# Performance work log

Hardware: AMD Instinct MI355X
Metric: run time of the kernel (lower is better)

Reference implementation:

```python
import jax, jax.numpy as jnp
import numpy as np

B, F, H, K, E = 512, 1280, 2560, 8, 9  # batch, feat_dim, 2*feat_dim, branching, n_internal
# Tree: root=node 0 (expert 0); level-1 nodes 1..8 (experts 1..8); level-2 leaves 9..72.

def setup_inputs() -> dict:
    key = jax.random.key(0)
    k0, k1, k2, k3, k4 = jax.random.split(key, 5)
    x = jax.random.normal(k0, (B, F), dtype=jnp.float32)
    W1 = jax.random.normal(k1, (E, F, H), dtype=jnp.float32) / np.sqrt(F)
    b1 = jnp.zeros((E, H), dtype=jnp.float32)
    W2 = jax.random.normal(k2, (E, H, K), dtype=jnp.float32) / np.sqrt(H)
    b2 = jnp.zeros((E, K), dtype=jnp.float32)
    return {"x": x, "W1": W1, "b1": b1, "W2": W2, "b2": b2}

def reference(x, W1, b1, W2, b2):
    # Batched experts: Linear(F->H) -> ReLU -> Linear(H->K), softmax over children.
    h = jax.nn.relu(jnp.einsum('bf,efh->ebh', x, W1) + b1[:, None, :])  # [E,B,H]
    logits = jnp.einsum('ebh,ehk->ebk', h, W2) + b2[:, None, :]          # [E,B,K]
    probs = jax.nn.softmax(logits, axis=-1)                              # [E,B,K]
    # Path products root->node for every node (matches leaf_probs in torch code).
    p0 = jnp.ones((1, x.shape[0]), dtype=x.dtype)        # root: prob 1        [1,B]
    p1 = probs[0].T                                       # nodes 1..8          [K,B]
    # leaves 9..72: parent of node n is 1+(n-9)//K, child index (n-9)%K
    p2 = (p1[:, None, :] * jnp.transpose(probs[1:E], (0, 2, 1))).reshape(K * K, -1)  # [64,B]
    leaf_probs = jnp.concatenate([p0, p1, p2], axis=0).T  # [B, 73]
    return leaf_probs, logits
```

## Files before the change

### kernel.cpp

```cpp
#include <hip/hip_runtime.h>

#define TB 512
#define TF 1280
#define TH 2560
#define TK 8
#define TE 9
#define SLOT 16384
#define BUFSZ 65536

typedef unsigned short ushortT;
typedef unsigned long long u64;
typedef __attribute__((ext_vector_type(8))) short short8;
typedef __attribute__((ext_vector_type(4))) short short4v;
typedef __attribute__((ext_vector_type(4))) float floatx4;

__device__ __forceinline__ unsigned short f2bf(float f) {
  union { float f; unsigned u; } v; v.f = f;
  unsigned r = v.u + 0x7fffu + ((v.u >> 16) & 1u);
  return (unsigned short)(r >> 16);
}

__device__ __forceinline__ unsigned pk2(float a, float b) {
  union { float f; unsigned u; } ua, ub; ua.f = a; ub.f = b;
  unsigned ra = ua.u + 0x7fffu + ((ua.u >> 16) & 1u);
  unsigned rb = ub.u + 0x7fffu + ((ub.u >> 16) & 1u);
  return __builtin_amdgcn_perm(rb, ra, 0x07060302);
}

__device__ __forceinline__ void gl_lds16(const void* g, void* l) {
  __builtin_amdgcn_global_load_lds(
      (const __attribute__((address_space(1))) unsigned*)g,
      (__attribute__((address_space(3))) unsigned*)l, 16, 0, 0);
}

__device__ __forceinline__ int swz(int o) { return o ^ (((o >> 7) & 7) << 4); }

__global__ __launch_bounds__(256) void prep_all(
    const float* __restrict__ x, const float* __restrict__ W1,
    const float* __restrict__ W2,
    char* __restrict__ Apk, ushortT* __restrict__ W2t, char* __restrict__ W1p) {
  const int b = blockIdx.x;
  const int t = threadIdx.x;
  if (b < 3600) {
    __shared__ ushortT Ts[256 * 40];
    const int khalf = b & 1;
    const int kt = (b >> 1) % 20;
    const int nt = ((b >> 1) / 20) % 10;
    const int e = b / 400;
    const int kbase = kt * 64 + khalf * 32;
    const int nbase = nt * 256;
    const int kr = t >> 6, n4 = (t & 63) * 4;
#pragma unroll
    for (int kk = 0; kk < 8; ++kk) {
      const int k2 = kk * 4 + kr;
      floatx4 v = *(const floatx4*)(W1 + ((long)e * TF + kbase + k2) * TH + nbase + n4);
#pragma unroll
      for (int i = 0; i < 4; ++i) Ts[(n4 + i) * 40 + k2] = f2bf(v[i]);
    }
    __syncthreads();
    char* dstbase = W1p + (long)b * SLOT;
#pragma unroll
    for (int p = 0; p < 4; ++p) {
      const int op = (p * 256 + t) * 16;
      const int o = swz(op);
      const int r = o >> 6, k2c = (o & 63) >> 1;
      short8 v = *(const short8*)&Ts[r * 40 + k2c];
      *(short8*)(dstbase + op) = v;
    }
  } else if (b < 3920) {
    const int i = (b - 3600) * 256 + t;
    const int cc = i & 1023, slot = i >> 10;
    const int khalf = slot & 1, s2 = slot >> 1;
    const int kt = s2 % 20, mt = s2 / 20;
    const int op = cc * 16;
    const int o = swz(op);
    const int r = o >> 6, k2 = (o & 63) >> 1;
    const float* src = x + (long)(mt * 256 + r) * TF + kt * 64 + khalf * 32 + k2;
    floatx4 v0 = *(const floatx4*)(src);
    floatx4 v1 = *(const floatx4*)(src + 4);
    u64 q0 = (u64)pk2(v0.x, v0.y) | ((u64)pk2(v0.z, v0.w) << 32);
    u64 q1 = (u64)pk2(v1.x, v1.y) | ((u64)pk2(v1.z, v1.w) << 32);
    *(ulonglong2*)(Apk + (long)i * 16) = make_ulonglong2(q0, q1);
  } else {
    const int o = (b - 3920) * 256 + t;
    if (o < TE * TK * TH) {
      const int hcol = o % TH;
      const int rest = o / TH;
      const int n = rest & 7;
      const int e = rest >> 3;
      W2t[(long)(e * TK + n) * TH + hcol] = f2bf(W2[((long)e * TH + hcol) * TK + n]);
    }
  }
}

__global__ __launch_bounds__(256) void prepass(
    const float* __restrict__ x, const float* __restrict__ W2,
    u64* __restrict__ xq, ushortT* __restrict__ W2t) {
  const int i = blockIdx.x * 256 + threadIdx.x;
  if (i < 320 * 512) {
    const int kq = i >> 9, m = i & 511;
    floatx4 v = *(const floatx4*)(x + (long)m * TF + kq * 4);
    xq[i] = (u64)pk2(v.x, v.y) | ((u64)pk2(v.z, v.w) << 32);
  } else {
    const int o = i - 320 * 512;
    if (o < TE * TK * TH) {
      const int hcol = o % TH;
      const int rest = o / TH;
      const int n = rest & 7;
      const int e = rest >> 3;
      W2t[(long)(e * TK + n) * TH + hcol] = f2bf(W2[((long)e * TH + hcol) * TK + n]);
    }
  }
}

__global__ __launch_bounds__(512, 2) void gemm1_8p(
    const char* __restrict__ Apk, const char* __restrict__ Bpk,
    const float* __restrict__ b1, ushortT* __restrict__ h) {
  __shared__ __align__(16) char lds[131072];
  const int t = threadIdx.x;
  const int lane = t & 63, w = t >> 6;
  const int wm = w >> 2, wn = w & 3;
  const int lm = lane & 15, lq = lane >> 4;
  const int bid = blockIdx.x;
  const int e = bid / 20;
  const int rem = bid % 20;
  const int nt = rem >> 1, mt = rem & 1;

  const char* Ab = Apk + (long)(mt * 20) * 2 * SLOT;
  const char* Bb = Bpk + (long)((e * 10 + nt) * 20) * 2 * SLOT;

  int oA[8], oB[4];
#pragma unroll
  for (int mi = 0; mi < 8; ++mi)
    oA[mi] = swz((wm * 128 + mi * 16 + lm) * 64 + lq * 16);
#pragma unroll
  for (int ni = 0; ni < 4; ++ni)
    oB[ni] = swz((wn * 64 + ni * 16 + lm) * 64 + lq * 16);

  auto STAGE = [&](int tile, int half) {
    if (tile >= 20) return;
    const char* src = (half & 1)
        ? Bb + (long)(tile * 2 + (half >> 1)) * SLOT
        : Ab + (long)(tile * 2 + (half >> 1)) * SLOT;
    char* dst = lds + (tile & 1) * BUFSZ + half * SLOT + w * 1024;
    gl_lds16(src + t * 16, dst);
    gl_lds16(src + 8192 + t * 16, dst + 8192);
  };

  floatx4 acc[8][4];
#pragma unroll
  for (int i = 0; i < 8; ++i)
#pragma unroll
    for (int j = 0; j < 4; ++j) acc[i][j] = (floatx4){0.f, 0.f, 0.f, 0.f};

  STAGE(0, 0); STAGE(0, 1); STAGE(0, 2); STAGE(0, 3);
  STAGE(1, 0); STAGE(1, 1); STAGE(1, 2);
  asm volatile("s_waitcnt vmcnt(6)" ::: "memory");
  __builtin_amdgcn_s_barrier();

  for (int j = 0; j < 20; ++j) {
    const char* buf = lds + (j & 1) * BUFSZ;
    short8 af[8], bfA, bfB;
#pragma unroll
    for (int mi = 0; mi < 8; ++mi)
      af[mi] = *(const short8*)(buf + 0 * SLOT + oA[mi]);
    bfA = *(const short8*)(buf + 1 * SLOT + oB[0]);
    bfB = *(const short8*)(buf + 1 * SLOT + oB[1]);
    STAGE(j + 1, 3);
    __builtin_amdgcn_s_barrier();
    asm volatile("s_waitcnt lgkmcnt(0)" ::: "memory");
    __builtin_amdgcn_sched_barrier(0);
    __builtin_amdgcn_s_setprio(1);
#pragma unroll
    for (int mi = 0; mi < 8; ++mi) {
      acc[mi][0] = __builtin_amdgcn_mfma_f32_16x16x32_bf16(af[mi], bfA, acc[mi][0], 0, 0, 0);
      acc[mi][1] = __builtin_amdgcn_mfma_f32_16x16x32_bf16(af[mi], bfB, acc[mi][1], 0, 0, 0);
    }
    __builtin_amdgcn_s_setprio(0);
    __builtin_amdgcn_s_barrier();
    bfA = *(const short8*)(buf + 1 * SLOT + oB[2]);
    bfB = *(const short8*)(buf + 1 * SLOT + oB[3]);
    STAGE(j + 2, 0);
    __builtin_amdgcn_s_barrier();
    asm volatile("s_waitcnt lgkmcnt(0)" ::: "memory");
    __builtin_amdgcn_sched_barrier(0);
    __builtin_amdgcn_s_setprio(1);
#pragma unroll
    for (int mi = 0; mi < 8; ++mi) {
      acc[mi][2] = __builtin_amdgcn_mfma_f32_16x16x32_bf16(af[mi], bfA, acc[mi][2], 0, 0, 0);
      acc[mi][3] = __builtin_amdgcn_mfma_f32_16x16x32_bf16(af[mi], bfB, acc[mi][3], 0, 0, 0);
    }
    __builtin_amdgcn_s_setprio(0);
    __builtin_amdgcn_s_barrier();
#pragma unroll
    for (int mi = 0; mi < 8; ++mi)
      af[mi] = *(const short8*)(buf + 2 * SLOT + oA[mi]);
    bfA = *(const short8*)(buf + 3 * SLOT + oB[0]);
    bfB = *(const short8*)(buf + 3 * SLOT + oB[1]);
    STAGE(j + 2, 1);
    __builtin_amdgcn_s_barrier();
    asm volatile("s_waitcnt lgkmcnt(0)" ::: "memory");
    __builtin_amdgcn_sched_barrier(0);
    __builtin_amdgcn_s_setprio(1);
#pragma unroll
    for (int mi = 0; mi < 8; ++mi) {
      acc[mi][0] = __builtin_amdgcn_mfma_f32_16x16x32_bf16(af[mi], bfA, acc[mi][0], 0, 0, 0);
      acc[mi][1] = __builtin_amdgcn_mfma_f32_16x16x32_bf16(af[mi], bfB, acc[mi][1], 0, 0, 0);
    }
    __builtin_amdgcn_s_setprio(0);
    __builtin_amdgcn_s_barrier();
    bfA = *(const short8*)(buf + 3 * SLOT + oB[2]);
    bfB = *(const short8*)(buf + 3 * SLOT + oB[3]);
    STAGE(j + 2, 2);
    asm volatile("s_waitcnt vmcnt(6)" ::: "memory");
    __builtin_amdgcn_s_barrier();
    asm volatile("s_waitcnt lgkmcnt(0)" ::: "memory");
    __builtin_amdgcn_sched_barrier(0);
    __builtin_amdgcn_s_setprio(1);
#pragma unroll
    for (int mi = 0; mi < 8; ++mi) {
      acc[mi][2] = __builtin_amdgcn_mfma_f32_16x16x32_bf16(af[mi], bfA, acc[mi][2], 0, 0, 0);
      acc[mi][3] = __builtin_amdgcn_mfma_f32_16x16x32_bf16(af[mi], bfB, acc[mi][3], 0, 0, 0);
    }
    __builtin_amdgcn_s_setprio(0);
    __builtin_amdgcn_s_barrier();
  }

  const int rowbase = mt * 256 + wm * 128 + lq * 4;
  const int colbase = nt * 256 + wn * 64 + lm;
#pragma unroll
  for (int mi = 0; mi < 8; ++mi) {
    const int row = rowbase + mi * 16;
#pragma unroll
    for (int ni = 0; ni < 4; ++ni) {
      const int col = colbase + ni * 16;
      const float bias = b1[e * TH + col];
      floatx4 c = acc[mi][ni];
#pragma unroll
      for (int r = 0; r < 4; ++r) {
        float v = c[r] + bias;
        v = v > 0.f ? v : 0.f;
        h[((long)e * TB + row + r) * TH + col] = f2bf(v);
      }
    }
  }
}

__global__ __launch_bounds__(256) void gemm1_fb(
    const float* __restrict__ x, const float* __restrict__ W1,
    const float* __restrict__ b1, ushortT* __restrict__ h) {
  __shared__ __align__(16) ushortT As[128 * 40];
  __shared__ __align__(16) ushortT Bs[128 * 40];
  const int t = threadIdx.x;
  const int tileN = blockIdx.x;
  const int e = tileN / 20;
  const int hbase = (tileN % 20) * 128;
  const int m0 = blockIdx.y * 128;
  const int lane = t & 63, w = t >> 6;
  const int wm = w & 1, wn = w >> 1;
  const int lm = lane & 15, lq = lane >> 4;
  const int lk = lq * 8;
  floatx4 acc[4][4];
#pragma unroll
  for (int i = 0; i < 4; ++i)
#pragma unroll
    for (int j = 0; j < 4; ++j) acc[i][j] = (floatx4){0.f, 0.f, 0.f, 0.f};
  const float* wp = W1 + (long)e * TF * TH + hbase;
  const int cA = (t & 7) * 4;
  const int mA = t >> 3;
  const int nB = t & 127;
  const int gB = t >> 7;
  for (int kt = 0; kt < TF / 32; ++kt) {
    const int k0 = kt * 32;
    if (kt) __syncthreads();
#pragma unroll
    for (int i = 0; i < 4; ++i) {
      const int m = mA + 32 * i;
      floatx4 v = *(const floatx4*)(x + (long)(m0 + m) * TF + k0 + cA);
      short4v s; s.x = f2bf(v.x); s.y = f2bf(v.y); s.z = f2bf(v.z); s.w = f2bf(v.w);
      *(short4v*)&As[m * 40 + cA] = s;
    }
    {
      const float* bp = wp + (long)k0 * TH + nB;
#pragma unroll
      for (int q = 0; q < 4; ++q) {
        const int k4 = gB * 16 + q * 4;
        float f0 = bp[(long)(k4 + 0) * TH];
        float f1 = bp[(long)(k4 + 1) * TH];
        float f2 = bp[(long)(k4 + 2) * TH];
        float f3 = bp[(long)(k4 + 3) * TH];
        short4v s; s.x = f2bf(f0); s.y = f2bf(f1); s.z = f2bf(f2); s.w = f2bf(f3);
        *(short4v*)&Bs[nB * 40 + k4] = s;
      }
    }
    __syncthreads();
    short8 af[4], bfr[4];
#pragma unroll
    for (int mg = 0; mg < 4; ++mg)
      af[mg] = *(const short8*)&As[(wm * 64 + mg * 16 + lm) * 40 + lk];
#pragma unroll
    for (int ng = 0; ng < 4; ++ng)
      bfr[ng] = *(const short8*)&Bs[(wn * 64 + ng * 16 + lm) * 40 + lk];
#pragma unroll
    for (int mg = 0; mg < 4; ++mg)
#pragma unroll
      for (int ng = 0; ng < 4; ++ng)
        acc[mg][ng] = __builtin_amdgcn_mfma_f32_16x16x32_bf16(af[mg], bfr[ng], acc[mg][ng], 0, 0, 0);
  }
#pragma unroll
  for (int mg = 0; mg < 4; ++mg) {
    const int row = m0 + wm * 64 + mg * 16 + lq * 4;
#pragma unroll
    for (int ng = 0; ng < 4; ++ng) {
      const int col = hbase + wn * 64 + ng * 16 + lm;
      const float bias = b1[e * TH + col];
      floatx4 c = acc[mg][ng];
#pragma unroll
      for (int r = 0; r < 4; ++r) {
        float v = c[r] + bias;
        v = v > 0.f ? v : 0.f;
        h[((long)e * TB + row + r) * TH + col] = f2bf(v);
      }
    }
  }
}

__global__ __launch_bounds__(512) void gemm2_softmax(
    const ushortT* __restrict__ h, const ushortT* __restrict__ W2t,
    const float* __restrict__ b2, float* __restrict__ logits_out,
    float* __restrict__ probs) {
  __shared__ float Ls[8][16][8];
  const int t = threadIdx.x;
  const int lane = t & 63, w = t >> 6;
  const int e = blockIdx.x >> 5;
  const int r0 = (blockIdx.x & 31) * 16;
  const int lm = lane & 15, lq = lane >> 4;

  const ushortT* hp = h + ((long)(e * TB + r0 + lm)) * TH + w * 320 + lq * 8;
  const int bn = lm < 8 ? lm : 7;
  const ushortT* wp = W2t + ((long)(e * TK + bn)) * TH + w * 320 + lq * 8;

  floatx4 acc = (floatx4){0.f, 0.f, 0.f, 0.f};
#pragma unroll
  for (int kt = 0; kt < 10; ++kt) {
    short8 a = *(const short8*)(hp + kt * 32);
    short8 b = *(const short8*)(wp + kt * 32);
    acc = __builtin_amdgcn_mfma_f32_16x16x32_bf16(a, b, acc, 0, 0, 0);
  }
  if (lm < 8) {
#pragma unroll
    for (int r = 0; r < 4; ++r) Ls[w][lq * 4 + r][lm] = acc[r];
  }
  __syncthreads();
  if (w == 0 && lm < 8) {
    const float bias = b2[e * TK + lm];
#pragma unroll
    for (int r = 0; r < 4; ++r) {
      const int row = lq * 4 + r;
      float v = Ls[0][row][lm] + Ls[1][row][lm] + Ls[2][row][lm] + Ls[3][row][lm]
              + Ls[4][row][lm] + Ls[5][row][lm] + Ls[6][row][lm] + Ls[7][row][lm]
              + bias;
      float mx = v;
      mx = fmaxf(mx, __shfl_xor(mx, 1, 64));
      mx = fmaxf(mx, __shfl_xor(mx, 2, 64));
      mx = fmaxf(mx, __shfl_xor(mx, 4, 64));
      float ex = __expf(v - mx);
      float sm = ex;
      sm += __shfl_xor(sm, 1, 64);
      sm += __shfl_xor(sm, 2, 64);
      sm += __shfl_xor(sm, 4, 64);
      const long idx = ((long)e * TB + r0 + row) * TK + lm;
      logits_out[idx] = v;
      probs[idx] = ex / sm;
    }
  }
}

__global__ __launch_bounds__(256) void leafk(const float* __restrict__ probs,
                                             float* __restrict__ out) {
  const int idx = blockIdx.x * 256 + threadIdx.x;
  if (idx >= TB * 73) return;
  const int b = idx / 73, c = idx % 73;
  float v;
  if (c == 0) {
    v = 1.0f;
  } else if (c < 9) {
    v = probs[(long)b * TK + (c - 1)];
  } else {
    const int i = (c - 9) >> 3, j = (c - 9) & 7;
    v = probs[(long)b * TK + i] * probs[((long)(1 + i) * TB + b) * TK + j];
  }
  out[idx] = v;
}

extern "C" void kernel_launch(void* const* d_in, const int* in_sizes, int n_in,
                              void* d_out, int out_size, void* d_ws, size_t ws_size,
                              hipStream_t stream) {
  const float* x  = (const float*)d_in[0];
  const float* W1 = (const float*)d_in[1];
  const float* b1 = (const float*)d_in[2];
  const float* W2 = (const float*)d_in[3];
  const float* b2 = (const float*)d_in[4];
  float* out = (float*)d_out;

  ushortT* h     = (ushortT*)d_ws;
  float*   probs = (float*)((char*)d_ws + 23592960);
  char*    Apk   = (char*)d_ws + 23740416;
  ushortT* W2t   = (ushortT*)((char*)d_ws + 25051136);
  char*    W1p   = (char*)d_ws + 25419776;
  const size_t NEED = 25419776 + 58982400;
  float* logits_out = out + TB * 73;

  if (ws_size >= NEED) {
    prep_all<<<4640, 256, 0, stream>>>(x, W1, W2, Apk, W2t, W1p);
    gemm1_8p<<<180, 512, 0, stream>>>(Apk, W1p, b1, h);
  } else {
    prepass<<<1360, 256, 0, stream>>>(x, W2, (u64*)Apk, W2t);
    gemm1_fb<<<dim3(180, 4), 256, 0, stream>>>(x, W1, b1, h);
  }
  gemm2_softmax<<<TE * 32, 512, 0, stream>>>(h, W2t, b2, logits_out, probs);
  leafk<<<(TB * 73 + 255) / 256, 256, 0, stream>>>(probs, out);
}
```

Before: 235.6 us.

## Fuse second GEMM into first GEMM epilogue with atomic logit accumulation

The first GEMM epilogue now writes the ReLU'd bf16 tile to LDS and multiplies it by the W2 slice with MFMA, accumulating partial logits into a zeroed fp32 buffer via atomicAdd. This removes the write and re-read of the large hidden tensor h and the separate gemm2_softmax and leaf kernels, which a small finish kernel replaces by doing softmax and path products. In exchange it adds atomics across 10 N-tiles per output, non-deterministic summation order, extra zeroing blocks in the prep kernel and a full vmcnt drain in the last iterations.

```diff
diff --git a/kernel.cpp b/kernel.cpp
--- a/kernel.cpp
+++ b/kernel.cpp
@@ -38,7 +38,8 @@
 __global__ __launch_bounds__(256) void prep_all(
     const float* __restrict__ x, const float* __restrict__ W1,
     const float* __restrict__ W2,
-    char* __restrict__ Apk, ushortT* __restrict__ W2t, char* __restrict__ W1p) {
+    char* __restrict__ Apk, ushortT* __restrict__ W2t, char* __restrict__ W1p,
+    float* __restrict__ lacc) {
   const int b = blockIdx.x;
   const int t = threadIdx.x;
   if (b < 3600) {
@@ -81,7 +82,7 @@
     u64 q0 = (u64)pk2(v0.x, v0.y) | ((u64)pk2(v0.z, v0.w) << 32);
     u64 q1 = (u64)pk2(v1.x, v1.y) | ((u64)pk2(v1.z, v1.w) << 32);
     *(ulonglong2*)(Apk + (long)i * 16) = make_ulonglong2(q0, q1);
-  } else {
+  } else if (b < 4640) {
     const int o = (b - 3920) * 256 + t;
     if (o < TE * TK * TH) {
       const int hcol = o % TH;
@@ -90,6 +91,10 @@
       const int e = rest >> 3;
       W2t[(long)(e * TK + n) * TH + hcol] = f2bf(W2[((long)e * TH + hcol) * TK + n]);
     }
+  } else {
+    const int i = ((b - 4640) * 256 + t) * 4;
+    if (i < TE * TB * TK)
+      *(floatx4*)(lacc + i) = (floatx4){0.f, 0.f, 0.f, 0.f};
   }
 }
 
@@ -113,9 +118,10 @@
   }
 }
 
-__global__ __launch_bounds__(512, 2) void gemm1_8p(
+__global__ __launch_bounds__(512, 2) void gemm1_fused(
     const char* __restrict__ Apk, const char* __restrict__ Bpk,
-    const float* __restrict__ b1, ushortT* __restrict__ h) {
+    const float* __restrict__ b1, const ushortT* __restrict__ W2t,
+    float* __restrict__ lacc) {
   __shared__ __align__(16) char lds[131072];
   const int t = threadIdx.x;
   const int lane = t & 63, w = t >> 6;
@@ -212,7 +218,11 @@
     bfA = *(const short8*)(buf + 3 * SLOT + oB[2]);
     bfB = *(const short8*)(buf + 3 * SLOT + oB[3]);
     STAGE(j + 2, 2);
-    asm volatile("s_waitcnt vmcnt(6)" ::: "memory");
+    if (j >= 18) {
+      asm volatile("s_waitcnt vmcnt(0)" ::: "memory");
+    } else {
+      asm volatile("s_waitcnt vmcnt(6)" ::: "memory");
+    }
     __builtin_amdgcn_s_barrier();
     asm volatile("s_waitcnt lgkmcnt(0)" ::: "memory");
     __builtin_amdgcn_sched_barrier(0);
@@ -226,24 +236,94 @@
     __builtin_amdgcn_s_barrier();
   }
 
-  const int rowbase = mt * 256 + wm * 128 + lq * 4;
-  const int colbase = nt * 256 + wn * 64 + lm;
-#pragma unroll
-  for (int mi = 0; mi < 8; ++mi) {
-    const int row = rowbase + mi * 16;
-#pragma unroll
-    for (int ni = 0; ni < 4; ++ni) {
-      const int col = colbase + ni * 16;
-      const float bias = b1[e * TH + col];
+  short8 bq[8];
+  {
+    const ushortT* wp = W2t + ((long)(e * TK + (lm < 8 ? lm : 0))) * TH
+                        + nt * 256 + lq * 8;
+#pragma unroll
+    for (int kk = 0; kk < 8; ++kk) bq[kk] = *(const short8*)(wp + kk * 32);
+    if (lm >= 8) {
+#pragma unroll
+      for (int kk = 0; kk < 8; ++kk) bq[kk] = (short8)0;
+    }
+  }
+
+#pragma unroll
+  for (int ni = 0; ni < 4; ++ni) {
+    const int lcol = wn * 64 + ni * 16 + lm;
+    const float bias = b1[e * TH + nt * 256 + lcol];
+#pragma unroll
+    for (int mi = 0; mi < 8; ++mi) {
+      const int lr0 = wm * 128 + mi * 16 + lq * 4;
       floatx4 c = acc[mi][ni];
 #pragma unroll
       for (int r = 0; r < 4; ++r) {
         float v = c[r] + bias;
         v = v > 0.f ? v : 0.f;
-        h[((long)e * TB + row + r) * TH + col] = f2bf(v);
+        const int lrow = lr0 + r;
+        const int o = (lrow * 512 + lcol * 2) ^ ((lrow & 7) << 4);
+        *(ushortT*)(lds + o) = f2bf(v);
       }
     }
   }
+  __syncthreads();
+
+  floatx4 acc2[2];
+  acc2[0] = (floatx4){0.f, 0.f, 0.f, 0.f};
+  acc2[1] = (floatx4){0.f, 0.f, 0.f, 0.f};
+#pragma unroll
+  for (int rt = 0; rt < 2; ++rt) {
+    const int row = (w * 2 + rt) * 16 + lm;
+    const int rowb = row * 512;
+    const int sx = (row & 7) << 4;
+#pragma unroll
+    for (int kk = 0; kk < 8; ++kk) {
+      short8 a = *(const short8*)(lds + ((rowb + kk * 64 + lq * 16) ^ sx));
+      acc2[rt] = __builtin_amdgcn_mfma_f32_16x16x32_bf16(a, bq[kk], acc2[rt], 0, 0, 0);
+    }
+  }
+  if (lm < 8) {
+#pragma unroll
+    for (int rt = 0; rt < 2; ++rt) {
+      const int growb = mt * 256 + (w * 2 + rt) * 16 + lq * 4;
+#pragma unroll
+      for (int r = 0; r < 4; ++r)
+        atomicAdd(&lacc[((long)e * TB + growb + r) * TK + lm], acc2[rt][r]);
+    }
+  }
+}
+
+__global__ __launch_bounds__(256) void finish(
+    const float* __restrict__ lacc, const float* __restrict__ b2,
+    float* __restrict__ out, float* __restrict__ logits_out) {
+  const int b = blockIdx.x * 256 + threadIdx.x;
+  if (b >= TB) return;
+  float pr[TE][TK];
+#pragma unroll
+  for (int e = 0; e < TE; ++e) {
+    float lg[TK];
+    float mx = -1e30f;
+#pragma unroll
+    for (int k = 0; k < TK; ++k) {
+      lg[k] = lacc[((long)e * TB + b) * TK + k] + b2[e * TK + k];
+      logits_out[((long)e * TB + b) * TK + k] = lg[k];
+      mx = fmaxf(mx, lg[k]);
+    }
+    float sm = 0.f;
+#pragma unroll
+    for (int k = 0; k < TK; ++k) { pr[e][k] = __expf(lg[k] - mx); sm += pr[e][k]; }
+    const float inv = 1.f / sm;
+#pragma unroll
+    for (int k = 0; k < TK; ++k) pr[e][k] *= inv;
+  }
+  float* op = out + (long)b * 73;
+  op[0] = 1.0f;
+#pragma unroll
+  for (int i = 0; i < 8; ++i) op[1 + i] = pr[0][i];
+#pragma unroll
+  for (int i = 0; i < 8; ++i)
+#pragma unroll
+    for (int j = 0; j < 8; ++j) op[9 + i * 8 + j] = pr[0][i] * pr[1 + i][j];
 }
 
 __global__ __launch_bounds__(256) void gemm1_fb(
@@ -404,7 +484,7 @@
   float* out = (float*)d_out;
 
   ushortT* h     = (ushortT*)d_ws;
-  float*   probs = (float*)((char*)d_ws + 23592960);
+  float*   lacc  = (float*)((char*)d_ws + 23592960);
   char*    Apk   = (char*)d_ws + 23740416;
   ushortT* W2t   = (ushortT*)((char*)d_ws + 25051136);
   char*    W1p   = (char*)d_ws + 25419776;
@@ -412,12 +492,13 @@
   float* logits_out = out + TB * 73;
 
   if (ws_size >= NEED) {
-    prep_all<<<4640, 256, 0, stream>>>(x, W1, W2, Apk, W2t, W1p);
-    gemm1_8p<<<180, 512, 0, stream>>>(Apk, W1p, b1, h);
+    prep_all<<<4676, 256, 0, stream>>>(x, W1, W2, Apk, W2t, W1p, lacc);
+    gemm1_fused<<<180, 512, 0, stream>>>(Apk, W1p, b1, W2t, lacc);
+    finish<<<2, 256, 0, stream>>>(lacc, b2, out, logits_out);
   } else {
     prepass<<<1360, 256, 0, stream>>>(x, W2, (u64*)Apk, W2t);
     gemm1_fb<<<dim3(180, 4), 256, 0, stream>>>(x, W1, b1, h);
-  }
-  gemm2_softmax<<<TE * 32, 512, 0, stream>>>(h, W2t, b2, logits_out, probs);
-  leafk<<<(TB * 73 + 255) / 256, 256, 0, stream>>>(probs, out);
-}
+    gemm2_softmax<<<TE * 32, 512, 0, stream>>>(h, W2t, b2, logits_out, lacc);
+    leafk<<<(TB * 73 + 255) / 256, 256, 0, stream>>>(lacc, out);
+  }
+}
```

Result: no change. 232.7 us (-1.2%).
